# Performance work log

Hardware: AMD Instinct MI355X
Metric: run time of the kernel (lower is better)

The kernel has to match this reference:

```python
import jax, jax.numpy as jnp
import numpy as np

B, N, K = 4, 8192, 32
C_IN, C_MID, C_OUT = 64, 64, 128


def _uniform(key, shape, fan_in):
    s = 1.0 / np.sqrt(fan_in).astype(np.float32)
    return jax.random.uniform(key, shape, minval=-s, maxval=s, dtype=jnp.float32)


def setup_inputs() -> dict:
    key = jax.random.key(0)
    ks = jax.random.split(key, 8)
    p = jax.random.normal(ks[0], (B, N, 3), dtype=jnp.float32)
    f = jax.random.normal(ks[1], (B, C_IN, N), dtype=jnp.float32)
    dp = jax.random.normal(ks[2], (B, 3, N, K), dtype=jnp.float32)
    fj = jax.random.normal(ks[3], (B, C_IN, N, K), dtype=jnp.float32)
    # Conv2d 1x1 weights (PyTorch default kaiming-uniform-ish fan-in init)
    W1 = _uniform(ks[4], (C_MID, C_IN + 3), C_IN + 3)
    b1 = _uniform(ks[5], (C_MID,), C_IN + 3)
    W2 = _uniform(ks[6], (C_OUT, C_MID), C_MID)
    b2 = _uniform(ks[7], (C_OUT,), C_MID)
    return {"p": p, "f": f, "dp": dp, "fj": fj, "W1": W1, "b1": b1, "W2": W2, "b2": b2}


def reference(p, f, dp, fj, W1, b1, W2, b2):
    # fj <- cat([dp, fj], dim=1): [B, 3+C_in, N, K]
    x = jnp.concatenate([dp, fj], axis=1)
    # 1x1 Conv2d + ReLU (norm is None in source), layer 1: [B, C_mid, N, K]
    h = jax.nn.relu(jnp.einsum('oc,bcnk->bonk', W1, x) + b1[None, :, None, None])
    # layer 2 (use_res=False, is_head=False -> ReLU on last layer too): [B, C_out, N, K]
    h = jax.nn.relu(jnp.einsum('oc,bcnk->bonk', W2, h) + b2[None, :, None, None])
    # max-pool over neighbor axis K: [B, C_out, N]
    return jnp.max(h, axis=-1)
```

## Files before the change

kernel.cpp:

```cpp
#include <hip/hip_runtime.h>
#include <hip/hip_bf16.h>
#include <stdint.h>

#define B_    4
#define N_    8192
#define K_    32
#define CX    67
#define CMID  64
#define COUT  128

#define W1S   104
#define W2S   72
#define TPG   4
#define NWG   2048
#define GMAX  8191

#define W1E   (64 * W1S)
#define HB0   (W1E + 128 * W2S)
#define SMEME (HB0 + 4 * 32 * W2S)

typedef __bf16 bf16_t;
typedef bf16_t bf16x8 __attribute__((ext_vector_type(8)));
typedef float  f32x4  __attribute__((ext_vector_type(4)));

__device__ __forceinline__ uint32_t pack2bf(float a, float b) {
    union { bf16_t h[2]; uint32_t u; } x;
    x.h[0] = (bf16_t)a; x.h[1] = (bf16_t)b;
    return x.u;
}

template<bool DIRECT>
__global__ __launch_bounds__(256, 3)
void sa_main(const float* __restrict__ dp, const float* __restrict__ fj,
             const float* __restrict__ W1, const float* __restrict__ b1,
             const float* __restrict__ W2, const float* __restrict__ b2,
             float* __restrict__ dst)
{
    __shared__ bf16_t smem[SMEME];

    const int tid  = threadIdx.x;
    const int wave = tid >> 6;
    const int lane = tid & 63;
    const int lrow = lane & 15;
    const int g    = lane >> 4;

    const size_t plane = (size_t)N_ * K_;
    const int bidx = blockIdx.x;
    const int b    = (bidx * TPG) >> 11;

    const float* dpb = dp + (size_t)b * 3  * plane;
    const float* fjb = fj + (size_t)b * 64 * plane;

    const float* baseA = (g == 0) ? dpb
                       : fjb + (ptrdiff_t)(8 * g - 3) * (ptrdiff_t)plane;
    const float* baseB = fjb + (ptrdiff_t)(8 * g - 3) * (ptrdiff_t)plane;
    const float* base1 = fjb + (size_t)(29 + 8 * g) * plane;
    const float* base2 = fjb + (size_t)61 * plane;

    float la[19], lb[19];
    auto issue = [&](int G) {
        const int n = ((G & 2047) << 2) + wave;
        const size_t off = (size_t)n * K_ + lrow;
        const float* pA = baseA + off;
        const float* pB = baseB + off;
        const float* p1 = base1 + off;
        #pragma unroll
        for (int e = 0; e < 3; ++e) { la[e]   = pA[(size_t)e * plane]; lb[e]   = pA[(size_t)e * plane + 16]; }
        #pragma unroll
        for (int e = 3; e < 8; ++e) { la[e]   = pB[(size_t)e * plane]; lb[e]   = pB[(size_t)e * plane + 16]; }
        #pragma unroll
        for (int e = 0; e < 8; ++e) { la[8+e] = p1[(size_t)e * plane]; lb[8+e] = p1[(size_t)e * plane + 16]; }
        la[16] = la[17] = la[18] = 0.f;
        lb[16] = lb[17] = lb[18] = 0.f;
        if (g == 0) {
            const float* p2 = base2 + off;
            #pragma unroll
            for (int e = 0; e < 3; ++e) { la[16+e] = p2[(size_t)e * plane]; lb[16+e] = p2[(size_t)e * plane + 16]; }
        }
    };

    issue(bidx * TPG);

    for (int i = tid; i < W1E; i += 256) {
        int o = i / W1S, c = i - o * W1S;
        smem[i] = (c < CX) ? (bf16_t)W1[o * CX + c] : (bf16_t)0.f;
    }
    for (int i = tid; i < 128 * W2S; i += 256) {
        int o = i / W2S, c = i - o * W2S;
        smem[W1E + i] = (c < CMID) ? (bf16_t)W2[o * CMID + c] : (bf16_t)0.f;
    }
    __syncthreads();

    f32x4 b1f[4];
    #pragma unroll
    for (int rt = 0; rt < 4; ++rt) b1f[rt] = *(const f32x4*)(b1 + rt * 16 + g * 4);
    float b2f[8];
    #pragma unroll
    for (int ot = 0; ot < 8; ++ot) b2f[ot] = b2[ot * 16 + lrow];

    bf16_t* Hw = smem + HB0 + wave * 32 * W2S;
    const bf16_t* W2l = smem + W1E;

    #pragma unroll 1
    for (int t = 0; t < TPG; ++t) {
        const int G = bidx * TPG + t;
        const int n = ((G & 2047) << 2) + wave;

        bf16x8 f0[3], f1[3];
        {
            union { uint32_t u[4]; bf16x8 v; } cv;
            cv.u[0] = pack2bf(la[0], la[1]);   cv.u[1] = pack2bf(la[2], la[3]);
            cv.u[2] = pack2bf(la[4], la[5]);   cv.u[3] = pack2bf(la[6], la[7]);   f0[0] = cv.v;
            cv.u[0] = pack2bf(la[8], la[9]);   cv.u[1] = pack2bf(la[10], la[11]);
            cv.u[2] = pack2bf(la[12], la[13]); cv.u[3] = pack2bf(la[14], la[15]); f0[1] = cv.v;
            cv.u[0] = pack2bf(la[16], la[17]); cv.u[1] = pack2bf(la[18], 0.f);
            cv.u[2] = 0;                       cv.u[3] = 0;                       f0[2] = cv.v;
            cv.u[0] = pack2bf(lb[0], lb[1]);   cv.u[1] = pack2bf(lb[2], lb[3]);
            cv.u[2] = pack2bf(lb[4], lb[5]);   cv.u[3] = pack2bf(lb[6], lb[7]);   f1[0] = cv.v;
            cv.u[0] = pack2bf(lb[8], lb[9]);   cv.u[1] = pack2bf(lb[10], lb[11]);
            cv.u[2] = pack2bf(lb[12], lb[13]); cv.u[3] = pack2bf(lb[14], lb[15]); f1[1] = cv.v;
            cv.u[0] = pack2bf(lb[16], lb[17]); cv.u[1] = pack2bf(lb[18], 0.f);
            cv.u[2] = 0;                       cv.u[3] = 0;                       f1[2] = cv.v;
        }
        { int Gn = G + 1; if (Gn > GMAX) Gn = GMAX; issue(Gn); }

        f32x4 acc0[4] = {}, acc1v[4] = {};
        __builtin_amdgcn_s_setprio(1);
        #pragma unroll
        for (int kc = 0; kc < 3; ++kc) {
            #pragma unroll
            for (int rt = 0; rt < 4; ++rt) {
                bf16x8 wf = *(const bf16x8*)&smem[(rt * 16 + lrow) * W1S + kc * 32 + g * 8];
                acc0[rt]  = __builtin_amdgcn_mfma_f32_16x16x32_bf16(wf, f0[kc], acc0[rt], 0, 0, 0);
                acc1v[rt] = __builtin_amdgcn_mfma_f32_16x16x32_bf16(wf, f1[kc], acc1v[rt], 0, 0, 0);
            }
        }
        __builtin_amdgcn_s_setprio(0);

        #pragma unroll
        for (int rt = 0; rt < 4; ++rt) {
            float h0 = fmaxf(acc0[rt][0] + b1f[rt][0], 0.f);
            float h1 = fmaxf(acc0[rt][1] + b1f[rt][1], 0.f);
            float h2 = fmaxf(acc0[rt][2] + b1f[rt][2], 0.f);
            float h3 = fmaxf(acc0[rt][3] + b1f[rt][3], 0.f);
            *(uint2*)&Hw[lrow * W2S + rt * 16 + g * 4] =
                make_uint2(pack2bf(h0, h1), pack2bf(h2, h3));
            float j0 = fmaxf(acc1v[rt][0] + b1f[rt][0], 0.f);
            float j1 = fmaxf(acc1v[rt][1] + b1f[rt][1], 0.f);
            float j2 = fmaxf(acc1v[rt][2] + b1f[rt][2], 0.f);
            float j3 = fmaxf(acc1v[rt][3] + b1f[rt][3], 0.f);
            *(uint2*)&Hw[(16 + lrow) * W2S + rt * 16 + g * 4] =
                make_uint2(pack2bf(j0, j1), pack2bf(j2, j3));
        }

        bf16x8 hb00 = *(const bf16x8*)&Hw[lrow * W2S + g * 8];
        bf16x8 hb01 = *(const bf16x8*)&Hw[lrow * W2S + 32 + g * 8];
        bf16x8 hb10 = *(const bf16x8*)&Hw[(16 + lrow) * W2S + g * 8];
        bf16x8 hb11 = *(const bf16x8*)&Hw[(16 + lrow) * W2S + 32 + g * 8];

        float macc[8];
        __builtin_amdgcn_s_setprio(1);
        #pragma unroll
        for (int bt = 0; bt < 2; ++bt) {
            f32x4 a20[4] = {}, a21[4] = {};
            #pragma unroll
            for (int o = 0; o < 4; ++o) {
                #pragma unroll
                for (int kc2 = 0; kc2 < 2; ++kc2) {
                    bf16x8 wf = *(const bf16x8*)&W2l[((bt * 4 + o) * 16 + lrow) * W2S + kc2 * 32 + g * 8];
                    if (kc2 == 0) {
                        a20[o] = __builtin_amdgcn_mfma_f32_16x16x32_bf16(hb00, wf, a20[o], 0, 0, 0);
                        a21[o] = __builtin_amdgcn_mfma_f32_16x16x32_bf16(hb10, wf, a21[o], 0, 0, 0);
                    } else {
                        a20[o] = __builtin_amdgcn_mfma_f32_16x16x32_bf16(hb01, wf, a20[o], 0, 0, 0);
                        a21[o] = __builtin_amdgcn_mfma_f32_16x16x32_bf16(hb11, wf, a21[o], 0, 0, 0);
                    }
                }
            }
            #pragma unroll
            for (int o = 0; o < 4; ++o) {
                float m0 = fmaxf(fmaxf(a20[o][0], a20[o][1]), fmaxf(a20[o][2], a20[o][3]));
                float m1 = fmaxf(fmaxf(a21[o][0], a21[o][1]), fmaxf(a21[o][2], a21[o][3]));
                macc[bt * 4 + o] = fmaxf(m0, m1);
            }
        }
        __builtin_amdgcn_s_setprio(0);

        #pragma unroll
        for (int ot = 0; ot < 8; ++ot) {
            float vv = macc[ot];
            vv = fmaxf(vv, __shfl_xor(vv, 16, 64));
            vv = fmaxf(vv, __shfl_xor(vv, 32, 64));
            macc[ot] = fmaxf(vv + b2f[ot], 0.f);
        }
        float oa = (g == 0) ? macc[0] : (g == 1) ? macc[2] : (g == 2) ? macc[4] : macc[6];
        float ob = (g == 0) ? macc[1] : (g == 1) ? macc[3] : (g == 2) ? macc[5] : macc[7];
        const int ca = g * 32 + lrow;
        const int cb = g * 32 + 16 + lrow;
        if (DIRECT) {
            float* op = dst + (size_t)b * COUT * N_ + n;
            op[(size_t)ca * N_] = oa;
            op[(size_t)cb * N_] = ob;
        } else {
            float* wp = dst + ((size_t)(b * N_ + n)) * COUT;
            wp[ca] = oa;
            wp[cb] = ob;
        }
    }
}

__global__ __launch_bounds__(256)
void sa_transpose(const float* __restrict__ ws, float* __restrict__ out)
{
    __shared__ float tile[32][136];
    const int t  = threadIdx.x;
    const int i  = blockIdx.x;
    const int b  = i >> 8;
    const int n0 = (i & 255) << 5;

    const float* rp = ws + ((size_t)(b * N_ + n0)) * COUT;
    #pragma unroll
    for (int r = 0; r < 4; ++r) {
        int flat = (r * 256 + t) * 4;
        int nl = flat >> 7, c = flat & 127;
        float4 v = *(const float4*)(rp + (size_t)nl * COUT + c);
        *(float4*)&tile[nl][c] = v;
    }
    __syncthreads();
    float* op = out + (size_t)b * COUT * N_ + n0;
    const int nl4 = (t & 7) << 2;
    #pragma unroll
    for (int r2 = 0; r2 < 4; ++r2) {
        int c = r2 * 32 + (t >> 3);
        float4 o4;
        o4.x = tile[nl4 + 0][c];
        o4.y = tile[nl4 + 1][c];
        o4.z = tile[nl4 + 2][c];
        o4.w = tile[nl4 + 3][c];
        *(float4*)(op + (size_t)c * N_ + nl4) = o4;
    }
}

extern "C" void kernel_launch(void* const* d_in, const int* in_sizes, int n_in,
                              void* d_out, int out_size, void* d_ws, size_t ws_size,
                              hipStream_t stream) {
    const float* dp = (const float*)d_in[2];
    const float* fj = (const float*)d_in[3];
    const float* W1 = (const float*)d_in[4];
    const float* b1 = (const float*)d_in[5];
    const float* W2 = (const float*)d_in[6];
    const float* b2 = (const float*)d_in[7];
    float* out = (float*)d_out;

    const size_t ws_need = (size_t)B_ * N_ * COUT * sizeof(float);
    if (ws_size >= ws_need) {
        float* ws = (float*)d_ws;
        hipLaunchKernelGGL((sa_main<false>), dim3(NWG), dim3(256), 0, stream,
                           dp, fj, W1, b1, W2, b2, ws);
        hipLaunchKernelGGL(sa_transpose, dim3(1024), dim3(256), 0, stream, ws, out);
    } else {
        hipLaunchKernelGGL((sa_main<true>), dim3(NWG), dim3(256), 0, stream,
                           dp, fj, W1, b1, W2, b2, out);
    }
}
```

Before: 120.7 us.

## Keep layer-1 activations in registers via permuted W1 rows; float2 loads, double-buffered prefetch

Permutes the W1 row order in shared memory, along with the matching b1 indexing, so the layer-1 MFMA accumulator layout lines up directly with the B-operand fragment layout for layer 2. The hidden activations can then be packed in registers, which drops the per-wave LDS staging buffer and its write/read round trip. Global loads switch to float2 per lane covering two adjacent K entries. Two prefetch buffers now alternate across points, so loads run two points ahead. The cost is more register pressure, which could hurt occupancy at 3 waves per SIMD.

```diff
diff --git a/kernel.cpp b/kernel.cpp
--- a/kernel.cpp
+++ b/kernel.cpp
@@ -9,15 +9,14 @@
 #define CMID  64
 #define COUT  128
 
-#define W1S   104
+#define W1S   100
 #define W2S   72
 #define TPG   4
 #define NWG   2048
 #define GMAX  8191
 
 #define W1E   (64 * W1S)
-#define HB0   (W1E + 128 * W2S)
-#define SMEME (HB0 + 4 * 32 * W2S)
+#define SMEME (W1E + 128 * W2S)
 
 typedef __bf16 bf16_t;
 typedef bf16_t bf16x8 __attribute__((ext_vector_type(8)));
@@ -57,32 +56,37 @@
     const float* base1 = fjb + (size_t)(29 + 8 * g) * plane;
     const float* base2 = fjb + (size_t)61 * plane;
 
-    float la[19], lb[19];
-    auto issue = [&](int G) {
+    float2 la[16], la2[3], lb[16], lb2[3];
+    auto issue = [&](float2 (&v)[16], float2 (&v2)[3], int G) {
         const int n = ((G & 2047) << 2) + wave;
-        const size_t off = (size_t)n * K_ + lrow;
+        const size_t off = (size_t)n * K_ + 2 * lrow;
         const float* pA = baseA + off;
         const float* pB = baseB + off;
         const float* p1 = base1 + off;
         #pragma unroll
-        for (int e = 0; e < 3; ++e) { la[e]   = pA[(size_t)e * plane]; lb[e]   = pA[(size_t)e * plane + 16]; }
-        #pragma unroll
-        for (int e = 3; e < 8; ++e) { la[e]   = pB[(size_t)e * plane]; lb[e]   = pB[(size_t)e * plane + 16]; }
-        #pragma unroll
-        for (int e = 0; e < 8; ++e) { la[8+e] = p1[(size_t)e * plane]; lb[8+e] = p1[(size_t)e * plane + 16]; }
-        la[16] = la[17] = la[18] = 0.f;
-        lb[16] = lb[17] = lb[18] = 0.f;
+        for (int e = 0; e < 3; ++e) v[e]     = *(const float2*)(pA + (size_t)e * plane);
+        #pragma unroll
+        for (int e = 3; e < 8; ++e) v[e]     = *(const float2*)(pB + (size_t)e * plane);
+        #pragma unroll
+        for (int e = 0; e < 8; ++e) v[8 + e] = *(const float2*)(p1 + (size_t)e * plane);
+        v2[0] = v2[1] = v2[2] = make_float2(0.f, 0.f);
         if (g == 0) {
             const float* p2 = base2 + off;
             #pragma unroll
-            for (int e = 0; e < 3; ++e) { la[16+e] = p2[(size_t)e * plane]; lb[16+e] = p2[(size_t)e * plane + 16]; }
+            for (int e = 0; e < 3; ++e) v2[e] = *(const float2*)(p2 + (size_t)e * plane);
         }
     };
 
-    issue(bidx * TPG);
+    {
+        const int G0 = bidx * TPG;
+        issue(la, la2, G0);
+        issue(lb, lb2, G0 + 1 > GMAX ? GMAX : G0 + 1);
+    }
 
     for (int i = tid; i < W1E; i += 256) {
-        int o = i / W1S, c = i - o * W1S;
+        int s = i / W1S, c = i - s * W1S;
+        int rt = s >> 4, r = s & 15, q = r >> 2, ii = r & 3;
+        int o = 32 * (rt >> 1) + 8 * q + 4 * (rt & 1) + ii;
         smem[i] = (c < CX) ? (bf16_t)W1[o * CX + c] : (bf16_t)0.f;
     }
     for (int i = tid; i < 128 * W2S; i += 256) {
@@ -93,36 +97,37 @@
 
     f32x4 b1f[4];
     #pragma unroll
-    for (int rt = 0; rt < 4; ++rt) b1f[rt] = *(const f32x4*)(b1 + rt * 16 + g * 4);
+    for (int rt = 0; rt < 4; ++rt)
+        b1f[rt] = *(const f32x4*)(b1 + 32 * (rt >> 1) + 8 * g + 4 * (rt & 1));
     float b2f[8];
     #pragma unroll
     for (int ot = 0; ot < 8; ++ot) b2f[ot] = b2[ot * 16 + lrow];
 
-    bf16_t* Hw = smem + HB0 + wave * 32 * W2S;
     const bf16_t* W2l = smem + W1E;
 
-    #pragma unroll 1
-    for (int t = 0; t < TPG; ++t) {
-        const int G = bidx * TPG + t;
+    auto point = [&](float2 (&v)[16], float2 (&v2)[3], int G) {
         const int n = ((G & 2047) << 2) + wave;
 
         bf16x8 f0[3], f1[3];
+        #pragma unroll
+        for (int kc = 0; kc < 2; ++kc) {
+            union { uint32_t u[4]; bf16x8 w; } c0, c1;
+            #pragma unroll
+            for (int p = 0; p < 4; ++p) {
+                c0.u[p] = pack2bf(v[kc * 8 + 2 * p].x, v[kc * 8 + 2 * p + 1].x);
+                c1.u[p] = pack2bf(v[kc * 8 + 2 * p].y, v[kc * 8 + 2 * p + 1].y);
+            }
+            f0[kc] = c0.w; f1[kc] = c1.w;
+        }
         {
-            union { uint32_t u[4]; bf16x8 v; } cv;
-            cv.u[0] = pack2bf(la[0], la[1]);   cv.u[1] = pack2bf(la[2], la[3]);
-            cv.u[2] = pack2bf(la[4], la[5]);   cv.u[3] = pack2bf(la[6], la[7]);   f0[0] = cv.v;
-            cv.u[0] = pack2bf(la[8], la[9]);   cv.u[1] = pack2bf(la[10], la[11]);
-            cv.u[2] = pack2bf(la[12], la[13]); cv.u[3] = pack2bf(la[14], la[15]); f0[1] = cv.v;
-            cv.u[0] = pack2bf(la[16], la[17]); cv.u[1] = pack2bf(la[18], 0.f);
-            cv.u[2] = 0;                       cv.u[3] = 0;                       f0[2] = cv.v;
-            cv.u[0] = pack2bf(lb[0], lb[1]);   cv.u[1] = pack2bf(lb[2], lb[3]);
-            cv.u[2] = pack2bf(lb[4], lb[5]);   cv.u[3] = pack2bf(lb[6], lb[7]);   f1[0] = cv.v;
-            cv.u[0] = pack2bf(lb[8], lb[9]);   cv.u[1] = pack2bf(lb[10], lb[11]);
-            cv.u[2] = pack2bf(lb[12], lb[13]); cv.u[3] = pack2bf(lb[14], lb[15]); f1[1] = cv.v;
-            cv.u[0] = pack2bf(lb[16], lb[17]); cv.u[1] = pack2bf(lb[18], 0.f);
-            cv.u[2] = 0;                       cv.u[3] = 0;                       f1[2] = cv.v;
-        }
-        { int Gn = G + 1; if (Gn > GMAX) Gn = GMAX; issue(Gn); }
+            union { uint32_t u[4]; bf16x8 w; } c0, c1;
+            c0.u[0] = pack2bf(v2[0].x, v2[1].x); c0.u[1] = pack2bf(v2[2].x, 0.f);
+            c0.u[2] = 0; c0.u[3] = 0;
+            c1.u[0] = pack2bf(v2[0].y, v2[1].y); c1.u[1] = pack2bf(v2[2].y, 0.f);
+            c1.u[2] = 0; c1.u[3] = 0;
+            f0[2] = c0.w; f1[2] = c1.w;
+        }
+        { int Gn = G + 2; if (Gn > GMAX) Gn = GMAX; issue(v, v2, Gn); }
 
         f32x4 acc0[4] = {}, acc1v[4] = {};
         __builtin_amdgcn_s_setprio(1);
@@ -137,52 +142,43 @@
         }
         __builtin_amdgcn_s_setprio(0);
 
-        #pragma unroll
-        for (int rt = 0; rt < 4; ++rt) {
-            float h0 = fmaxf(acc0[rt][0] + b1f[rt][0], 0.f);
-            float h1 = fmaxf(acc0[rt][1] + b1f[rt][1], 0.f);
-            float h2 = fmaxf(acc0[rt][2] + b1f[rt][2], 0.f);
-            float h3 = fmaxf(acc0[rt][3] + b1f[rt][3], 0.f);
-            *(uint2*)&Hw[lrow * W2S + rt * 16 + g * 4] =
-                make_uint2(pack2bf(h0, h1), pack2bf(h2, h3));
-            float j0 = fmaxf(acc1v[rt][0] + b1f[rt][0], 0.f);
-            float j1 = fmaxf(acc1v[rt][1] + b1f[rt][1], 0.f);
-            float j2 = fmaxf(acc1v[rt][2] + b1f[rt][2], 0.f);
-            float j3 = fmaxf(acc1v[rt][3] + b1f[rt][3], 0.f);
-            *(uint2*)&Hw[(16 + lrow) * W2S + rt * 16 + g * 4] =
-                make_uint2(pack2bf(j0, j1), pack2bf(j2, j3));
-        }
-
-        bf16x8 hb00 = *(const bf16x8*)&Hw[lrow * W2S + g * 8];
-        bf16x8 hb01 = *(const bf16x8*)&Hw[lrow * W2S + 32 + g * 8];
-        bf16x8 hb10 = *(const bf16x8*)&Hw[(16 + lrow) * W2S + g * 8];
-        bf16x8 hb11 = *(const bf16x8*)&Hw[(16 + lrow) * W2S + 32 + g * 8];
+        bf16x8 a2f0[2], a2f1[2];
+        #pragma unroll
+        for (int kc2 = 0; kc2 < 2; ++kc2) {
+            union { uint32_t u[4]; bf16x8 w; } c0, c1;
+            #pragma unroll
+            for (int hh = 0; hh < 2; ++hh) {
+                const int rt = 2 * kc2 + hh;
+                float h0 = fmaxf(acc0[rt][0] + b1f[rt][0], 0.f);
+                float h1 = fmaxf(acc0[rt][1] + b1f[rt][1], 0.f);
+                float h2 = fmaxf(acc0[rt][2] + b1f[rt][2], 0.f);
+                float h3 = fmaxf(acc0[rt][3] + b1f[rt][3], 0.f);
+                c0.u[hh * 2 + 0] = pack2bf(h0, h1);
+                c0.u[hh * 2 + 1] = pack2bf(h2, h3);
+                float j0 = fmaxf(acc1v[rt][0] + b1f[rt][0], 0.f);
+                float j1 = fmaxf(acc1v[rt][1] + b1f[rt][1], 0.f);
+                float j2 = fmaxf(acc1v[rt][2] + b1f[rt][2], 0.f);
+                float j3 = fmaxf(acc1v[rt][3] + b1f[rt][3], 0.f);
+                c1.u[hh * 2 + 0] = pack2bf(j0, j1);
+                c1.u[hh * 2 + 1] = pack2bf(j2, j3);
+            }
+            a2f0[kc2] = c0.w; a2f1[kc2] = c1.w;
+        }
 
         float macc[8];
         __builtin_amdgcn_s_setprio(1);
         #pragma unroll
-        for (int bt = 0; bt < 2; ++bt) {
-            f32x4 a20[4] = {}, a21[4] = {};
-            #pragma unroll
-            for (int o = 0; o < 4; ++o) {
-                #pragma unroll
-                for (int kc2 = 0; kc2 < 2; ++kc2) {
-                    bf16x8 wf = *(const bf16x8*)&W2l[((bt * 4 + o) * 16 + lrow) * W2S + kc2 * 32 + g * 8];
-                    if (kc2 == 0) {
-                        a20[o] = __builtin_amdgcn_mfma_f32_16x16x32_bf16(hb00, wf, a20[o], 0, 0, 0);
-                        a21[o] = __builtin_amdgcn_mfma_f32_16x16x32_bf16(hb10, wf, a21[o], 0, 0, 0);
-                    } else {
-                        a20[o] = __builtin_amdgcn_mfma_f32_16x16x32_bf16(hb01, wf, a20[o], 0, 0, 0);
-                        a21[o] = __builtin_amdgcn_mfma_f32_16x16x32_bf16(hb11, wf, a21[o], 0, 0, 0);
-                    }
-                }
-            }
-            #pragma unroll
-            for (int o = 0; o < 4; ++o) {
-                float m0 = fmaxf(fmaxf(a20[o][0], a20[o][1]), fmaxf(a20[o][2], a20[o][3]));
-                float m1 = fmaxf(fmaxf(a21[o][0], a21[o][1]), fmaxf(a21[o][2], a21[o][3]));
-                macc[bt * 4 + o] = fmaxf(m0, m1);
-            }
+        for (int ot = 0; ot < 8; ++ot) {
+            bf16x8 w20 = *(const bf16x8*)&W2l[(ot * 16 + lrow) * W2S +  0 + g * 8];
+            bf16x8 w21 = *(const bf16x8*)&W2l[(ot * 16 + lrow) * W2S + 32 + g * 8];
+            f32x4 t0 = {}, t1 = {};
+            t0 = __builtin_amdgcn_mfma_f32_16x16x32_bf16(a2f0[0], w20, t0, 0, 0, 0);
+            t0 = __builtin_amdgcn_mfma_f32_16x16x32_bf16(a2f0[1], w21, t0, 0, 0, 0);
+            t1 = __builtin_amdgcn_mfma_f32_16x16x32_bf16(a2f1[0], w20, t1, 0, 0, 0);
+            t1 = __builtin_amdgcn_mfma_f32_16x16x32_bf16(a2f1[1], w21, t1, 0, 0, 0);
+            float m0 = fmaxf(fmaxf(t0[0], t0[1]), fmaxf(t0[2], t0[3]));
+            float m1 = fmaxf(fmaxf(t1[0], t1[1]), fmaxf(t1[2], t1[3]));
+            macc[ot] = fmaxf(m0, m1);
         }
         __builtin_amdgcn_s_setprio(0);
 
@@ -206,6 +202,13 @@
             wp[ca] = oa;
             wp[cb] = ob;
         }
+    };
+
+    #pragma unroll 1
+    for (int t = 0; t < TPG; t += 2) {
+        const int G = bidx * TPG + t;
+        point(la, la2, G);
+        point(lb, lb2, G + 1);
     }
 }
 
```

New measurement: 187.5 us. 1.55x slower.
